# Optimization experiments

Hardware: AMD Instinct MI355X
Metric: run time of the kernel (lower is better)

The kernel has to match this reference:

```python
import jax, jax.numpy as jnp
import numpy as np

STEPS = 100
VTH = 1.0
POOL_TH = 0.75


def _conv(x, w):
    # 5x5 conv, stride 1, pad 2, no bias; NCHW / OIHW
    return jax.lax.conv_general_dilated(
        x, w, window_strides=(1, 1), padding=[(2, 2), (2, 2)],
        dimension_numbers=('NCHW', 'OIHW', 'NCHW'))


def _avgpool2(x):
    s = jax.lax.reduce_window(x, 0.0, jax.lax.add, (1, 1, 2, 2), (1, 1, 2, 2), 'VALID')
    return s * 0.25


def _fire(mem, th):
    # torch.nn.functional.threshold(mem, th, 0): keep values > th, else 0
    ex = jnp.where(mem > th, mem, 0.0)
    mem = mem - ex
    out = (ex > 0).astype(mem.dtype)
    return mem, out


def _ave(output, inp):
    c = inp >= output
    denom = jnp.sum(jnp.where(c, inp, 0.0))
    num = jnp.sum(jnp.where(c, output, 0.0))
    return jnp.where(denom < 1e-3, 1.0, num / denom)


def _ave_p(output, inp):
    denom = jnp.sum(inp)
    return jnp.where(denom < 1e-3, 1.0, jnp.sum(output) / denom)


def setup_inputs() -> dict:
    key = jax.random.key(0)
    k_in, k1, k2, k3, k4 = jax.random.split(key, 5)
    B = 512
    inputdata = jax.random.uniform(k_in, (B, 1, 28, 28), dtype=jnp.float32)
    w1 = jax.random.normal(k1, (20, 1, 5, 5), dtype=jnp.float32) * np.sqrt(2.0 / (5 * 5 * 1))
    w2 = jax.random.normal(k2, (50, 20, 5, 5), dtype=jnp.float32) * np.sqrt(2.0 / (5 * 5 * 20))
    wf0 = jax.random.normal(k3, (200, 2450), dtype=jnp.float32) * np.sqrt(2.0 / 2450)
    wf1 = jax.random.normal(k4, (10, 200), dtype=jnp.float32) * np.sqrt(2.0 / 200)
    return {'inputdata': inputdata, 'w1': w1, 'w2': w2, 'wf0': wf0, 'wf1': wf1}


def _spiking_loop(inputdata, w1, w2, wf0, wf1):
    B = inputdata.shape[0]
    f32 = jnp.float32
    z = lambda *s: jnp.zeros(s, f32)
    carry0 = (
        z(B, 20, 28, 28), z(B, 20, 14, 14), z(B, 50, 14, 14), z(B, 50, 7, 7), z(B, 200),  # membranes
        z(B, 1, 28, 28),                                                                   # Total_input
        z(B, 20, 28, 28), z(B, 20, 28, 28),   # Total_1_output, IF_in_c1
        z(B, 20, 14, 14), z(B, 20, 14, 14),   # Total_p1_output, IF_in_p1
        z(B, 50, 14, 14), z(B, 50, 14, 14),   # Total_2_output, IF_in_c2
        z(B, 50, 7, 7), z(B, 50, 7, 7),       # Total_p2_output, IF_in_p2
        z(B, 200), z(B, 200),                  # Total_f0_output, IF_in_f0
    )

    sgn = jnp.sign(inputdata)
    half = jnp.abs(inputdata) / 2.0

    def step(carry, k):
        (m1, m1s, m2, m2s, mf0, Tin, T1, IFc1, Tp1, IFp1, T2, IFc2, Tp2, IFp2, Tf0, IFf0) = carry
        r = jax.random.uniform(k, inputdata.shape, dtype=f32)
        poisson = (half > r).astype(f32) * sgn
        Tin = Tin + poisson

        a = _conv(poisson, w1)
        m1 = m1 + a
        m1, o = _fire(m1, VTH)            # LIF (l=1 -> membrane unchanged)
        IFc1 = IFc1 + a
        T1 = T1 + o

        a = _avgpool2(o)
        m1s = m1s + a
        m1s, o = _fire(m1s, POOL_TH)
        IFp1 = IFp1 + a
        Tp1 = Tp1 + o

        a = _conv(o, w2)
        m2 = m2 + a
        m2, o = _fire(m2, VTH)
        IFc2 = IFc2 + a
        T2 = T2 + o

        a = _avgpool2(o)
        m2s = m2s + a
        m2s, o = _fire(m2s, POOL_TH)
        IFp2 = IFp2 + a
        Tp2 = Tp2 + o

        a = o.reshape(B, -1) @ wf0.T
        mf0 = mf0 + a
        mf0, o = _fire(mf0, VTH)
        IFf0 = IFf0 + a
        Tf0 = Tf0 + o

        return (m1, m1s, m2, m2s, mf0, Tin, T1, IFc1, Tp1, IFp1, T2, IFc2, Tp2, IFp2, Tf0, IFf0), None

    keys = jax.random.split(jax.random.key(42), STEPS)
    carry, _ = jax.lax.scan(step, carry0, keys)
    return jax.lax.stop_gradient(carry)  # loop ran under torch.no_grad()


def _forward(inputdata, w1, w2, wf0, wf1):
    sg = jax.lax.stop_gradient
    (_, _, _, _, _, Tin, T1, IFc1, Tp1, IFp1, T2, IFc2, Tp2, IFp2, Tf0, IFf0) = \
        _spiking_loop(inputdata, w1, w2, wf0, wf1)

    # global scales start at 1, sign == 1 branch taken
    s1 = 0.6 * _ave(T1, IFc1) + 0.4
    s2 = 0.6 * _ave_p(Tp1, IFp1) + 0.4
    s3 = 0.6 * _ave(T2, IFc2) + 0.4
    s4 = 0.6 * _ave_p(Tp2, IFp2) + 0.4
    s5 = 0.6 * _ave(Tf0, IFf0) + 0.4
    sc1 = s1 * (IFc1 > 0).astype(jnp.float32)
    sc2 = s2 * (IFp1 > 0).astype(jnp.float32)
    sc3 = s3 * (IFc2 > 0).astype(jnp.float32)
    sc4 = s4 * (IFp2 > 0).astype(jnp.float32)
    sc5 = s5 * (IFf0 > 0).astype(jnp.float32)

    # straight-through graph (ASF-BP)
    B = inputdata.shape[0]
    o = _conv(Tin, w1) * sc1
    T1g = o - sg(o) + T1
    o = _avgpool2(T1g) * sc2
    Tp1g = o - sg(o) + Tp1
    o = _conv(Tp1g, w2) * sc3
    T2g = o - sg(o) + T2
    o = _avgpool2(T2g) * sc4
    Tp2g = o - sg(o) + Tp2
    o = (Tp2g.reshape(B, -1) @ wf0.T) * sc5
    Tf0g = o - sg(o) + Tf0
    fc1_in = Tf0g @ wf1.T
    return fc1_in / VTH / STEPS


def reference(inputdata, w1, w2, wf0, wf1):
    return _forward(inputdata, w1, w2, wf0, wf1)
```

## Files before the change

### kernel.cpp

```cpp
#include <hip/hip_runtime.h>
#include <stdint.h>

#define STEPS 100

typedef float f2 __attribute__((ext_vector_type(2)));

__device__ __forceinline__ uint32_t rotl32(uint32_t v, int r) {
  return (v << r) | (v >> (32 - r));
}

__device__ __forceinline__ void tf2x32(uint32_t k0, uint32_t k1,
                                       uint32_t x0, uint32_t x1,
                                       uint32_t& o0, uint32_t& o1) {
  uint32_t ks2 = k0 ^ k1 ^ 0x1BD11BDAu;
  x0 += k0; x1 += k1;
#define RND(r) { x0 += x1; x1 = rotl32(x1, (r)); x1 ^= x0; }
  RND(13) RND(15) RND(26) RND(6)
  x0 += k1;  x1 += ks2 + 1u;
  RND(17) RND(29) RND(16) RND(24)
  x0 += ks2; x1 += k0 + 2u;
  RND(13) RND(15) RND(26) RND(6)
  x0 += k0;  x1 += k1 + 3u;
  RND(17) RND(29) RND(16) RND(24)
  x0 += k1;  x1 += ks2 + 4u;
  RND(13) RND(15) RND(26) RND(6)
  x0 += ks2; x1 += k0 + 5u;
#undef RND
  o0 = x0; o1 = x1;
}

__global__ void keys_k(uint32_t* __restrict__ kb) {
  int i = threadIdx.x;
  if (i < STEPS) {
    uint32_t a, b;
    tf2x32(0u, 42u, 0u, (uint32_t)i, a, b);
    kb[2 * i] = a;
    kb[2 * i + 1] = b;
  }
}

__global__ void wt3_k(const float* __restrict__ w2, float* __restrict__ wT3) {
  int i = blockIdx.x * blockDim.x + threadIdx.x;
  if (i >= 50 * 20 * 72) return;
  int oc = i / 1440, r = i % 1440;
  int ic = r / 72, q = r % 72;
  int jr = q / 12, p = q % 12;
  float v = 0.f;
  if (p < 10) {
    int kx = p >> 1, h = p & 1;
    if (h == 0 && jr < 5)  v = w2[oc * 500 + ic * 25 + jr * 5 + kx];
    if (h == 1 && jr >= 1) v = w2[oc * 500 + ic * 25 + (jr - 1) * 5 + kx];
  }
  wT3[i] = v;
}

__global__ void wf0t_k(const float* __restrict__ wf0,
                       float* __restrict__ wf0T) {
  int i = blockIdx.x * blockDim.x + threadIdx.x;
  if (i >= 2450 * 256) return;
  int k = i >> 8, n = i & 255;
  wf0T[i] = (n < 200) ? wf0[n * 2450 + k] : 0.f;
}

__device__ __forceinline__ void p2blk(const float4& q0, const float4& q1,
                                      const float4& q2, const float4& q3,
                                      const f2* wp, f2* acc2) {
  float u[18] = {q0.x, q0.y, q0.z, q0.w, q1.x, q1.y, q1.z, q1.w,
                 q2.x, q2.y, q2.z, q2.w, q3.x, q3.y, q3.z, q3.w, 0.f, 0.f};
#pragma unroll
  for (int kx = 0; kx < 5; ++kx) {
    f2 w = wp[kx];
#pragma unroll
    for (int xx = 0; xx < 14; ++xx) {
      f2 us = {u[xx + kx], u[xx + kx]};
      acc2[xx] = __builtin_elementwise_fma(w, us, acc2[xx]);
    }
  }
}

__device__ __forceinline__ void ldwp(const float* wic, int jr, f2* wp) {
  const float4* p = reinterpret_cast<const float4*>(wic + jr * 12);
  float4 a = p[0], b = p[1];
  wp[0] = f2{a.x, a.y}; wp[1] = f2{a.z, a.w};
  wp[2] = f2{b.x, b.y}; wp[3] = f2{b.z, b.w};
  float2 c = *reinterpret_cast<const float2*>(wic + jr * 12 + 8);
  wp[4] = f2{c.x, c.y};
}

__global__ __launch_bounds__(512, 2) void step_all_k(
    const float* __restrict__ x, const float* __restrict__ w1,
    const float* __restrict__ wT3, const uint32_t* __restrict__ kb,
    uint32_t* __restrict__ sp2g) {
  __shared__ __align__(16) float  xhs_l[784];
  __shared__ __align__(16) float  pois_l[32 * 34];
  __shared__ __align__(16) float  sp1_l[20 * 18 * 20];
  __shared__ __align__(16) float  m2_l[50 * 196];
  __shared__ float    m2s_l[2450];
  __shared__ float    m1s_l[20 * 196];
  __shared__ float    m1stash[512 * 21];
  __shared__ uint8_t  fb[352];

  const int b  = blockIdx.x;
  const int t  = threadIdx.x;
  const int lq = t & 255;
  const int ohu = __builtin_amdgcn_readfirstlane(t >> 8);
  const bool act1 = lq < 196;
  const int qy = lq / 14, qx = lq % 14;
  const bool act2 = t < 350;
  const int oc2 = t / 7;
  const int rp  = t % 7;
  const int y0  = 2 * rp;

  for (int p = t; p < 784; p += 512) {
    xhs_l[p] = x[b * 784 + p] * 0.5f;
  }
  for (int i = t; i < 32 * 34; i += 512) pois_l[i] = 0.f;
  for (int i = t; i < 20 * 360; i += 512) sp1_l[i] = 0.f;
  for (int i = t; i < 50 * 196; i += 512) m2_l[i] = 0.f;
  for (int i = t; i < 2450; i += 512) m2s_l[i] = 0.f;
  for (int i = t; i < 20 * 196; i += 512) m1s_l[i] = 0.f;
  for (int i = t; i < 512 * 21; i += 512) m1stash[i] = 0.f;
  if (t < 352) fb[t] = 0;

  float m1p[2][10];
#pragma unroll
  for (int i = 0; i < 10; ++i) {
    m1p[0][i] = 0.f;
    m1p[1][i] = 0.f;
  }
  __syncthreads();

  {
    uint32_t k0 = kb[0], k1 = kb[1];
    for (int p = t; p < 784; p += 512) {
      uint32_t o0, o1;
      tf2x32(k0, k1, 0u, (uint32_t)(b * 784 + p), o0, o1);
      float r = __uint_as_float(((o0 ^ o1) >> 9) | 0x3F800000u) - 1.0f;
      float v = xhs_l[p];
      pois_l[(p / 28 + 2) * 34 + (p % 28 + 2)] =
          (fabsf(v) > r) ? ((v > 0.f) ? 1.f : -1.f) : 0.f;
    }
  }
  __syncthreads();

#define LDROW(rr, d) {                                                      \
    const float2* _pr = reinterpret_cast<const float2*>(                    \
        &pois_l[(2 * qy + (rr)) * 34 + 2 * qx]);                            \
    float2 _a0 = _pr[0], _a1 = _pr[1], _a2 = _pr[2];                        \
    d[0] = _a0.x; d[1] = _a0.y; d[2] = _a1.x;                               \
    d[3] = _a1.y; d[4] = _a2.x; d[5] = _a2.y; }

#define LD4(icv, jrv, p0, p1, p2, p3) {                                     \
    const float4* _rn = reinterpret_cast<const float4*>(                    \
        sp1_l + (icv) * 360 + (y0 + (jrv)) * 20);                           \
    p0 = _rn[0]; p1 = _rn[1]; p2 = _rn[2]; p3 = _rn[3]; }

  for (int s = 0; s < STEPS; ++s) {
    if (act1) {
      float rA[6], rB[6];
      LDROW(0, rA)
      LDROW(1, rB)
      float acc[4][10];
#pragma unroll
      for (int tt = 0; tt < 4; ++tt)
#pragma unroll
        for (int i = 0; i < 10; ++i) acc[tt][i] = 0.f;
#pragma unroll
      for (int ky = 0; ky < 5; ++ky) {
#pragma unroll
        for (int kx = 0; kx < 5; ++kx) {
#pragma unroll
          for (int i = 0; i < 10; ++i) {
            float w = w1[(ohu * 10 + i) * 25 + ky * 5 + kx];
            acc[0][i] += w * rA[kx];
            acc[1][i] += w * rA[kx + 1];
            acc[2][i] += w * rB[kx];
            acc[3][i] += w * rB[kx + 1];
          }
        }
        if (ky < 4) {
#pragma unroll
          for (int j = 0; j < 6; ++j) rA[j] = rB[j];
          LDROW(ky + 2, rB)
        }
      }
#pragma unroll
      for (int i = 0; i < 10; ++i) {
        float s4[4];
#pragma unroll
        for (int tt = 0; tt < 2; ++tt) {
          float m = m1p[tt][i] + acc[tt][i];
          float sp = 0.f;
          if (m > 1.0f) { sp = 1.f; m = 0.f; }
          m1p[tt][i] = m;
          s4[tt] = sp;
        }
        {
          float m = m1stash[t * 21 + i] + acc[2][i];
          float sp = 0.f;
          if (m > 1.0f) { sp = 1.f; m = 0.f; }
          m1stash[t * 21 + i] = m;
          s4[2] = sp;
        }
        {
          float m = m1stash[t * 21 + 10 + i] + acc[3][i];
          float sp = 0.f;
          if (m > 1.0f) { sp = 1.f; m = 0.f; }
          m1stash[t * 21 + 10 + i] = m;
          s4[3] = sp;
        }
        float a = 0.25f * (((s4[0] + s4[1]) + s4[2]) + s4[3]);
        int mi = (ohu * 10 + i) * 196 + lq;
        float mm = m1s_l[mi] + a;
        float spp = 0.f;
        if (mm > 0.75f) { spp = 1.f; mm = 0.f; }
        m1s_l[mi] = mm;
        sp1_l[(ohu * 10 + i) * 360 + (qy + 2) * 20 + (qx + 2)] = spp;
      }
    }
    __syncthreads();

    if (act2) {
      f2 acc2[14];
#pragma unroll
      for (int xx = 0; xx < 14; ++xx) acc2[xx] = f2{0.f, 0.f};
      const float* wb = wT3 + oc2 * 1440;
      float4 A0, A1, A2, A3, B0, B1, B2, B3;
      f2 W0[5], W1[5], W2[5];
      LD4(0, 0, A0, A1, A2, A3)
      ldwp(wb, 0, W0);
      LD4(0, 1, B0, B1, B2, B3)
      ldwp(wb, 1, W1);
      ldwp(wb, 2, W2);
#pragma unroll 1
      for (int ic = 0; ic < 20; ++ic) {
        const int icn = (ic < 19) ? ic + 1 : 19;
        const float* wic  = wb + ic * 72;
        const float* wicn = wb + icn * 72;
        p2blk(A0, A1, A2, A3, W0, acc2);
        LD4(ic, 2, A0, A1, A2, A3)
        ldwp(wic, 3, W0);
        __builtin_amdgcn_sched_barrier(0);
        p2blk(B0, B1, B2, B3, W1, acc2);
        LD4(ic, 3, B0, B1, B2, B3)
        ldwp(wic, 4, W1);
        __builtin_amdgcn_sched_barrier(0);
        p2blk(A0, A1, A2, A3, W2, acc2);
        LD4(ic, 4, A0, A1, A2, A3)
        ldwp(wic, 5, W2);
        __builtin_amdgcn_sched_barrier(0);
        p2blk(B0, B1, B2, B3, W0, acc2);
        LD4(ic, 5, B0, B1, B2, B3)
        ldwp(wicn, 0, W0);
        __builtin_amdgcn_sched_barrier(0);
        p2blk(A0, A1, A2, A3, W1, acc2);
        LD4(icn, 0, A0, A1, A2, A3)
        ldwp(wicn, 1, W1);
        __builtin_amdgcn_sched_barrier(0);
        p2blk(B0, B1, B2, B3, W2, acc2);
        LD4(icn, 1, B0, B1, B2, B3)
        ldwp(wicn, 2, W2);
        __builtin_amdgcn_sched_barrier(0);
      }
      float f0[14], f1[14];
#pragma unroll
      for (int xx = 0; xx < 14; ++xx) {
        int li = oc2 * 196 + y0 * 14 + xx;
        float m = m2_l[li] + acc2[xx].x;
        float sp = 0.f;
        if (m > 1.0f) { sp = 1.f; m = 0.f; }
        m2_l[li] = m;
        f0[xx] = sp;
      }
#pragma unroll
      for (int xx = 0; xx < 14; ++xx) {
        int li = oc2 * 196 + (y0 + 1) * 14 + xx;
        float m = m2_l[li] + acc2[xx].y;
        float sp = 0.f;
        if (m > 1.0f) { sp = 1.f; m = 0.f; }
        m2_l[li] = m;
        f1[xx] = sp;
      }
      uint32_t byte = 0;
#pragma unroll
      for (int xo = 0; xo < 7; ++xo) {
        float a = 0.25f * (((f0[2 * xo] + f0[2 * xo + 1]) + f1[2 * xo]) +
                           f1[2 * xo + 1]);
        int e = oc2 * 49 + rp * 7 + xo;
        float m = m2s_l[e] + a;
        uint32_t bit = 0;
        if (m > 0.75f) { bit = 1; m = 0.f; }
        m2s_l[e] = m;
        byte |= bit << xo;
      }
      fb[t] = (uint8_t)byte;
    } else if (t >= 384) {
      if (s + 1 < STEPS) {
        uint32_t k0 = kb[2 * (s + 1)], k1 = kb[2 * (s + 1) + 1];
        for (int p = t - 384; p < 784; p += 128) {
          uint32_t o0, o1;
          tf2x32(k0, k1, 0u, (uint32_t)(b * 784 + p), o0, o1);
          float r = __uint_as_float(((o0 ^ o1) >> 9) | 0x3F800000u) - 1.0f;
          float v = xhs_l[p];
          pois_l[(p / 28 + 2) * 34 + (p % 28 + 2)] =
              (fabsf(v) > r) ? ((v > 0.f) ? 1.f : -1.f) : 0.f;
        }
      }
    }
    __syncthreads();

    if (t < 77) {
      int j0 = (32 * t) / 7;
      uint64_t accw = 0;
#pragma unroll
      for (int jj = 0; jj < 6; ++jj) {
        int j = j0 + jj;
        uint32_t bv = (j < 350) ? (uint32_t)fb[j] : 0u;
        accw |= (uint64_t)bv << (7 * j - 32 * t + 6);
      }
      sp2g[b * 7700 + s * 77 + t] = (uint32_t)(accw >> 6);
    }
  }
#undef LDROW
#undef LD4
}

__global__ __launch_bounds__(256) void fc0f_k(
    const uint32_t* __restrict__ sp2g, const float* __restrict__ wf0T,
    float* __restrict__ Tf0g) {
  __shared__ uint32_t mk[77];
  const int b = blockIdx.x;
  const int n = threadIdx.x;
  float m = 0.f, T = 0.f;
  for (int s = 0; s < STEPS; ++s) {
    __syncthreads();
    if (n < 77) mk[n] = sp2g[b * 7700 + s * 77 + n];
    __syncthreads();
    float acc = 0.f;
    for (int d = 0; d < 77; ++d) {
      uint32_t um = mk[d];
      while (um) {
        int j = __builtin_ctz(um);
        um &= um - 1;
        acc += wf0T[((d << 5) + j) * 256 + n];
      }
    }
    m += acc;
    if (m > 1.0f) { T += 1.f; m = 0.f; }
  }
  if (n < 200) Tf0g[b * 200 + n] = T;
}

__global__ void fc1_k(const float* __restrict__ Tf0,
                      const float* __restrict__ wf1,
                      float* __restrict__ out) {
  int idx = blockIdx.x * blockDim.x + threadIdx.x;
  if (idx >= 5120) return;
  int b = idx / 10, i = idx % 10;
  float a = 0.f;
  for (int j = 0; j < 200; ++j) a += Tf0[b * 200 + j] * wf1[i * 200 + j];
  out[idx] = (a / 1.0f) / 100.0f;
}

extern "C" void kernel_launch(void* const* d_in, const int* in_sizes, int n_in,
                              void* d_out, int out_size, void* d_ws, size_t ws_size,
                              hipStream_t stream) {
  (void)in_sizes; (void)n_in; (void)out_size; (void)ws_size;
  const float* x   = (const float*)d_in[0];
  const float* w1  = (const float*)d_in[1];
  const float* w2  = (const float*)d_in[2];
  const float* wf0 = (const float*)d_in[3];
  const float* wf1 = (const float*)d_in[4];
  float* out = (float*)d_out;
  char* ws = (char*)d_ws;

  const size_t tf0_b  = 512ull * 200 * 4;
  const size_t wt_b   = 50ull * 20 * 72 * 4;
  const size_t key_b  = 1024;
  const size_t wf0t_b = 2450ull * 256 * 4;
  float*    Tf0g = (float*)ws;
  float*    wT3  = (float*)(ws + tf0_b);
  uint32_t* kb   = (uint32_t*)(ws + tf0_b + wt_b);
  float*    wf0T = (float*)(ws + tf0_b + wt_b + key_b);
  uint32_t* sp2g = (uint32_t*)(ws + tf0_b + wt_b + key_b + wf0t_b);

  keys_k<<<1, 128, 0, stream>>>(kb);
  wt3_k<<<282, 256, 0, stream>>>(w2, wT3);
  wf0t_k<<<2450, 256, 0, stream>>>(wf0, wf0T);
  step_all_k<<<512, 512, 0, stream>>>(x, w1, wT3, kb, sp2g);
  fc0f_k<<<512, 256, 0, stream>>>(sp2g, wf0T, Tf0g);
  fc1_k<<<20, 256, 0, stream>>>(Tf0g, wf1, out);
}
```

Before: 9.912 ms.

## Restructure conv2 inner loop to pack adjacent x outputs in f2 lanes

Conv2 accumulation changes from packing two output rows per f2 lane (which needed a zero-padded, duplicated 72-float weight layout) to packing two adjacent x columns per lane, with separate accumulators for each of the two rows. Weights are now a compact 28-float-per-channel array loaded once per input channel into registers, instead of being reloaded per row. Row contributions that fall outside the kernel are skipped at compile time, so fewer multiply-adds are issued. In exchange, register pressure rises (28 weight registers plus even and odd input pairs), and the weights are no longer prefetched into registers ahead of use.

```diff
diff --git a/kernel.cpp b/kernel.cpp
--- a/kernel.cpp
+++ b/kernel.cpp
@@ -39,19 +39,12 @@
   }
 }
 
-__global__ void wt3_k(const float* __restrict__ w2, float* __restrict__ wT3) {
+__global__ void wt_k(const float* __restrict__ w2, float* __restrict__ wT2) {
   int i = blockIdx.x * blockDim.x + threadIdx.x;
-  if (i >= 50 * 20 * 72) return;
-  int oc = i / 1440, r = i % 1440;
-  int ic = r / 72, q = r % 72;
-  int jr = q / 12, p = q % 12;
-  float v = 0.f;
-  if (p < 10) {
-    int kx = p >> 1, h = p & 1;
-    if (h == 0 && jr < 5)  v = w2[oc * 500 + ic * 25 + jr * 5 + kx];
-    if (h == 1 && jr >= 1) v = w2[oc * 500 + ic * 25 + (jr - 1) * 5 + kx];
-  }
-  wT3[i] = v;
+  if (i >= 50 * 560) return;
+  int oc = i / 560, r = i % 560;
+  int ic = r / 28, j = r % 28;
+  wT2[i] = (j < 25) ? w2[oc * 500 + ic * 25 + j] : 0.f;
 }
 
 __global__ void wf0t_k(const float* __restrict__ wf0,
@@ -62,34 +55,57 @@
   wf0T[i] = (n < 200) ? wf0[n * 2450 + k] : 0.f;
 }
 
-__device__ __forceinline__ void p2blk(const float4& q0, const float4& q1,
-                                      const float4& q2, const float4& q3,
-                                      const f2* wp, f2* acc2) {
-  float u[18] = {q0.x, q0.y, q0.z, q0.w, q1.x, q1.y, q1.z, q1.w,
-                 q2.x, q2.y, q2.z, q2.w, q3.x, q3.y, q3.z, q3.w, 0.f, 0.f};
-#pragma unroll
-  for (int kx = 0; kx < 5; ++kx) {
-    f2 w = wp[kx];
-#pragma unroll
-    for (int xx = 0; xx < 14; ++xx) {
-      f2 us = {u[xx + kx], u[xx + kx]};
-      acc2[xx] = __builtin_elementwise_fma(w, us, acc2[xx]);
-    }
-  }
-}
-
-__device__ __forceinline__ void ldwp(const float* wic, int jr, f2* wp) {
-  const float4* p = reinterpret_cast<const float4*>(wic + jr * 12);
-  float4 a = p[0], b = p[1];
-  wp[0] = f2{a.x, a.y}; wp[1] = f2{a.z, a.w};
-  wp[2] = f2{b.x, b.y}; wp[3] = f2{b.z, b.w};
-  float2 c = *reinterpret_cast<const float2*>(wic + jr * 12 + 8);
-  wp[4] = f2{c.x, c.y};
+template <int JR>
+__device__ __forceinline__ void p2x(const float4& q0, const float4& q1,
+                                    const float4& q2, const float4& q3,
+                                    const float (&wv)[28],
+                                    f2 (&a0)[7], f2 (&a1)[7]) {
+  f2 E[8] = {{q0.x, q0.y}, {q0.z, q0.w}, {q1.x, q1.y}, {q1.z, q1.w},
+             {q2.x, q2.y}, {q2.z, q2.w}, {q3.x, q3.y}, {q3.z, q3.w}};
+  f2 O[8] = {{q0.y, q0.z}, {q0.w, q1.x}, {q1.y, q1.z}, {q1.w, q2.x},
+             {q2.y, q2.z}, {q2.w, q3.x}, {q3.y, q3.z}, {q3.w, 0.f}};
+  if (JR < 5) {
+    f2 W;
+    W = f2{wv[JR * 5 + 0], wv[JR * 5 + 0]};
+#pragma unroll
+    for (int j = 0; j < 7; ++j) a0[j] = __builtin_elementwise_fma(W, E[j], a0[j]);
+    W = f2{wv[JR * 5 + 1], wv[JR * 5 + 1]};
+#pragma unroll
+    for (int j = 0; j < 7; ++j) a0[j] = __builtin_elementwise_fma(W, O[j], a0[j]);
+    W = f2{wv[JR * 5 + 2], wv[JR * 5 + 2]};
+#pragma unroll
+    for (int j = 0; j < 7; ++j) a0[j] = __builtin_elementwise_fma(W, E[j + 1], a0[j]);
+    W = f2{wv[JR * 5 + 3], wv[JR * 5 + 3]};
+#pragma unroll
+    for (int j = 0; j < 7; ++j) a0[j] = __builtin_elementwise_fma(W, O[j + 1], a0[j]);
+    W = f2{wv[JR * 5 + 4], wv[JR * 5 + 4]};
+#pragma unroll
+    for (int j = 0; j < 6; ++j) a0[j] = __builtin_elementwise_fma(W, E[j + 2], a0[j]);
+  }
+  if (JR >= 1) {
+    constexpr int K = (JR - 1) * 5;
+    f2 W;
+    W = f2{wv[K + 0], wv[K + 0]};
+#pragma unroll
+    for (int j = 0; j < 7; ++j) a1[j] = __builtin_elementwise_fma(W, E[j], a1[j]);
+    W = f2{wv[K + 1], wv[K + 1]};
+#pragma unroll
+    for (int j = 0; j < 7; ++j) a1[j] = __builtin_elementwise_fma(W, O[j], a1[j]);
+    W = f2{wv[K + 2], wv[K + 2]};
+#pragma unroll
+    for (int j = 0; j < 7; ++j) a1[j] = __builtin_elementwise_fma(W, E[j + 1], a1[j]);
+    W = f2{wv[K + 3], wv[K + 3]};
+#pragma unroll
+    for (int j = 0; j < 7; ++j) a1[j] = __builtin_elementwise_fma(W, O[j + 1], a1[j]);
+    W = f2{wv[K + 4], wv[K + 4]};
+#pragma unroll
+    for (int j = 0; j < 6; ++j) a1[j] = __builtin_elementwise_fma(W, E[j + 2], a1[j]);
+  }
 }
 
 __global__ __launch_bounds__(512, 2) void step_all_k(
     const float* __restrict__ x, const float* __restrict__ w1,
-    const float* __restrict__ wT3, const uint32_t* __restrict__ kb,
+    const float* __restrict__ wT2, const uint32_t* __restrict__ kb,
     uint32_t* __restrict__ sp2g) {
   __shared__ __align__(16) float  xhs_l[784];
   __shared__ __align__(16) float  pois_l[32 * 34];
@@ -221,65 +237,85 @@
     __syncthreads();
 
     if (act2) {
-      f2 acc2[14];
-#pragma unroll
-      for (int xx = 0; xx < 14; ++xx) acc2[xx] = f2{0.f, 0.f};
-      const float* wb = wT3 + oc2 * 1440;
+      f2 a0[7], a1[7];
+#pragma unroll
+      for (int j = 0; j < 7; ++j) { a0[j] = f2{0.f, 0.f}; a1[j] = f2{0.f, 0.f}; }
       float4 A0, A1, A2, A3, B0, B1, B2, B3;
-      f2 W0[5], W1[5], W2[5];
       LD4(0, 0, A0, A1, A2, A3)
-      ldwp(wb, 0, W0);
       LD4(0, 1, B0, B1, B2, B3)
-      ldwp(wb, 1, W1);
-      ldwp(wb, 2, W2);
 #pragma unroll 1
       for (int ic = 0; ic < 20; ++ic) {
         const int icn = (ic < 19) ? ic + 1 : 19;
-        const float* wic  = wb + ic * 72;
-        const float* wicn = wb + icn * 72;
-        p2blk(A0, A1, A2, A3, W0, acc2);
+        float wv[28];
+        {
+          const float4* wb4 =
+              reinterpret_cast<const float4*>(wT2 + oc2 * 560 + ic * 28);
+#pragma unroll
+          for (int j = 0; j < 7; ++j) {
+            float4 q = wb4[j];
+            wv[4 * j]     = q.x;
+            wv[4 * j + 1] = q.y;
+            wv[4 * j + 2] = q.z;
+            wv[4 * j + 3] = q.w;
+          }
+        }
+        p2x<0>(A0, A1, A2, A3, wv, a0, a1);
         LD4(ic, 2, A0, A1, A2, A3)
-        ldwp(wic, 3, W0);
-        __builtin_amdgcn_sched_barrier(0);
-        p2blk(B0, B1, B2, B3, W1, acc2);
+        __builtin_amdgcn_sched_barrier(0);
+        p2x<1>(B0, B1, B2, B3, wv, a0, a1);
         LD4(ic, 3, B0, B1, B2, B3)
-        ldwp(wic, 4, W1);
-        __builtin_amdgcn_sched_barrier(0);
-        p2blk(A0, A1, A2, A3, W2, acc2);
+        __builtin_amdgcn_sched_barrier(0);
+        p2x<2>(A0, A1, A2, A3, wv, a0, a1);
         LD4(ic, 4, A0, A1, A2, A3)
-        ldwp(wic, 5, W2);
-        __builtin_amdgcn_sched_barrier(0);
-        p2blk(B0, B1, B2, B3, W0, acc2);
+        __builtin_amdgcn_sched_barrier(0);
+        p2x<3>(B0, B1, B2, B3, wv, a0, a1);
         LD4(ic, 5, B0, B1, B2, B3)
-        ldwp(wicn, 0, W0);
-        __builtin_amdgcn_sched_barrier(0);
-        p2blk(A0, A1, A2, A3, W1, acc2);
+        __builtin_amdgcn_sched_barrier(0);
+        p2x<4>(A0, A1, A2, A3, wv, a0, a1);
         LD4(icn, 0, A0, A1, A2, A3)
-        ldwp(wicn, 1, W1);
-        __builtin_amdgcn_sched_barrier(0);
-        p2blk(B0, B1, B2, B3, W2, acc2);
+        __builtin_amdgcn_sched_barrier(0);
+        p2x<5>(B0, B1, B2, B3, wv, a0, a1);
         LD4(icn, 1, B0, B1, B2, B3)
-        ldwp(wicn, 2, W2);
         __builtin_amdgcn_sched_barrier(0);
       }
       float f0[14], f1[14];
 #pragma unroll
-      for (int xx = 0; xx < 14; ++xx) {
-        int li = oc2 * 196 + y0 * 14 + xx;
-        float m = m2_l[li] + acc2[xx].x;
-        float sp = 0.f;
-        if (m > 1.0f) { sp = 1.f; m = 0.f; }
-        m2_l[li] = m;
-        f0[xx] = sp;
-      }
-#pragma unroll
-      for (int xx = 0; xx < 14; ++xx) {
-        int li = oc2 * 196 + (y0 + 1) * 14 + xx;
-        float m = m2_l[li] + acc2[xx].y;
-        float sp = 0.f;
-        if (m > 1.0f) { sp = 1.f; m = 0.f; }
-        m2_l[li] = m;
-        f1[xx] = sp;
+      for (int j = 0; j < 7; ++j) {
+        {
+          int li = oc2 * 196 + y0 * 14 + 2 * j;
+          float m = m2_l[li] + a0[j].x;
+          float sp = 0.f;
+          if (m > 1.0f) { sp = 1.f; m = 0.f; }
+          m2_l[li] = m;
+          f0[2 * j] = sp;
+        }
+        {
+          int li = oc2 * 196 + y0 * 14 + 2 * j + 1;
+          float m = m2_l[li] + a0[j].y;
+          float sp = 0.f;
+          if (m > 1.0f) { sp = 1.f; m = 0.f; }
+          m2_l[li] = m;
+          f0[2 * j + 1] = sp;
+        }
+      }
+#pragma unroll
+      for (int j = 0; j < 7; ++j) {
+        {
+          int li = oc2 * 196 + (y0 + 1) * 14 + 2 * j;
+          float m = m2_l[li] + a1[j].x;
+          float sp = 0.f;
+          if (m > 1.0f) { sp = 1.f; m = 0.f; }
+          m2_l[li] = m;
+          f1[2 * j] = sp;
+        }
+        {
+          int li = oc2 * 196 + (y0 + 1) * 14 + 2 * j + 1;
+          float m = m2_l[li] + a1[j].y;
+          float sp = 0.f;
+          if (m > 1.0f) { sp = 1.f; m = 0.f; }
+          m2_l[li] = m;
+          f1[2 * j + 1] = sp;
+        }
       }
       uint32_t byte = 0;
 #pragma unroll
@@ -375,19 +411,19 @@
   char* ws = (char*)d_ws;
 
   const size_t tf0_b  = 512ull * 200 * 4;
-  const size_t wt_b   = 50ull * 20 * 72 * 4;
+  const size_t wt_b   = 50ull * 560 * 4;
   const size_t key_b  = 1024;
   const size_t wf0t_b = 2450ull * 256 * 4;
   float*    Tf0g = (float*)ws;
-  float*    wT3  = (float*)(ws + tf0_b);
+  float*    wT2  = (float*)(ws + tf0_b);
   uint32_t* kb   = (uint32_t*)(ws + tf0_b + wt_b);
   float*    wf0T = (float*)(ws + tf0_b + wt_b + key_b);
   uint32_t* sp2g = (uint32_t*)(ws + tf0_b + wt_b + key_b + wf0t_b);
 
   keys_k<<<1, 128, 0, stream>>>(kb);
-  wt3_k<<<282, 256, 0, stream>>>(w2, wT3);
+  wt_k<<<110, 256, 0, stream>>>(w2, wT2);
   wf0t_k<<<2450, 256, 0, stream>>>(wf0, wf0T);
-  step_all_k<<<512, 512, 0, stream>>>(x, w1, wT3, kb, sp2g);
+  step_all_k<<<512, 512, 0, stream>>>(x, w1, wT2, kb, sp2g);
   fc0f_k<<<512, 256, 0, stream>>>(sp2g, wf0T, Tf0g);
   fc1_k<<<20, 256, 0, stream>>>(Tf0g, wf1, out);
 }
```

After: 9.839 ms. Within noise of the previous version (-0.7%).
